# Performance work log

Measured on AMD Instinct MI355X. Metric: run time of the kernel, lower is better.

The kernel has to match this reference:

```python
import jax, jax.numpy as jnp
import numpy as np

H = 128          # h_dim
N_NODES = 100000
N_EDGES = 1600000
N_GRAPHS = 256
EPS_BN = 1e-5


def setup_inputs() -> dict:
    key = jax.random.key(0)
    ks = jax.random.split(key, 12)
    x = jax.random.normal(ks[0], (N_NODES, 4), dtype=jnp.float32)
    edge_index = jax.random.randint(ks[1], (2, N_EDGES), 0, N_NODES, dtype=jnp.int64)
    batch = jnp.sort(jax.random.randint(ks[2], (N_NODES,), 0, N_GRAPHS, dtype=jnp.int64))
    # Linear weights (xavier-ish scale), stored as [in, out]
    W1 = jax.random.normal(ks[3], (4, H), dtype=jnp.float32) * (1.0 / np.sqrt(4))
    W2 = jax.random.normal(ks[4], (H, H), dtype=jnp.float32) * (1.0 / np.sqrt(H))
    W3 = jax.random.normal(ks[5], (H, H), dtype=jnp.float32) * (1.0 / np.sqrt(H))
    Wfc = jax.random.normal(ks[6], (H, 1), dtype=jnp.float32) * (1.0 / np.sqrt(H))
    def bn_params(k):
        k1, k2, k3, k4 = jax.random.split(k, 4)
        gamma = 1.0 + 0.1 * jax.random.normal(k1, (H,), dtype=jnp.float32)
        beta = 0.1 * jax.random.normal(k2, (H,), dtype=jnp.float32)
        mean = 0.1 * jax.random.normal(k3, (H,), dtype=jnp.float32)
        var = 1.0 + 0.1 * jax.random.uniform(k4, (H,), dtype=jnp.float32)
        return gamma, beta, mean, var
    g1, b1, m1, v1 = bn_params(ks[7])
    g2, b2, m2, v2 = bn_params(ks[8])
    g3, b3, m3, v3 = bn_params(ks[9])
    return {
        "x": x, "edge_index": edge_index, "batch": batch,
        "W1": W1, "g1": g1, "b1": b1, "m1": m1, "v1": v1,
        "W2": W2, "g2": g2, "b2": b2, "m2": m2, "v2": v2,
        "W3": W3, "g3": g3, "b3": b3, "m3": m3, "v3": v3,
        "Wfc": Wfc,
    }


def _gin_layer(h, src, dst, W, gamma, beta, mean, var):
    # GINConv with eps=0: mlp(x + sum_{j in N(i)} x_j)
    aggr = jax.ops.segment_sum(h[src], dst, num_segments=N_NODES)
    z = (h + aggr) @ W                                  # Linear(bias=False)
    z = (z - mean) * (gamma / jnp.sqrt(var + EPS_BN)) + beta  # BatchNorm1d (eval)
    return jax.nn.relu(z)


def reference(x, edge_index, batch,
              W1, g1, b1, m1, v1,
              W2, g2, b2, m2, v2,
              W3, g3, b3, m3, v3,
              Wfc):
    src, dst = edge_index[0], edge_index[1]
    h = _gin_layer(x, src, dst, W1, g1, b1, m1, v1)
    h = _gin_layer(h, src, dst, W2, g2, b2, m2, v2)
    h = _gin_layer(h, src, dst, W3, g3, b3, m3, v3)
    # dropout: identity in eval mode
    sums = jax.ops.segment_sum(h, batch, num_segments=N_GRAPHS)      # [G, H]
    cnts = jax.ops.segment_sum(jnp.ones((N_NODES, 1), h.dtype), batch,
                               num_segments=N_GRAPHS)                # [G, 1]
    pooled = sums / jnp.maximum(cnts, 1.0)
    return jax.nn.sigmoid(pooled @ Wfc)                               # [G, 1]
```

## Files before the change

### kernel.cpp

```cpp
#include <hip/hip_runtime.h>
#include <hip/hip_fp8.h>
#include <math.h>

#define N_NODES 100000
#define N_EDGES 1600000
#define N_GRAPHS 256
#define H 128
#define EPS_BN 1e-5f
#define ELLW 64

#define PSZ 256
#define PSH 8
#define P_PART 391
#define BLD_NBLK 200
#define EPT 32
#define EPB_A (256 * EPT)

typedef unsigned int uint;
typedef unsigned short ushort;
typedef __attribute__((ext_vector_type(8))) short bf16x8;
typedef __attribute__((ext_vector_type(4))) float f32x4;
typedef __attribute__((ext_vector_type(2))) float f32x2;
typedef __attribute__((ext_vector_type(4))) int i32x4;
typedef __attribute__((ext_vector_type(2))) int i32x2;

__device__ __forceinline__ uint f2bf_bits(float x) {
    uint u = __float_as_uint(x);
    return (u + 0x7fffu + ((u >> 16) & 1u)) >> 16;
}
__device__ __forceinline__ uint pack_bf2(float a, float b) {
    return f2bf_bits(a) | (f2bf_bits(b) << 16);
}

__device__ __forceinline__ unsigned char f32_to_fp8(float x) {
#if __has_builtin(__builtin_amdgcn_cvt_pk_fp8_f32)
    int v = __builtin_amdgcn_cvt_pk_fp8_f32(x, 0.0f, 0, false);
    return (unsigned char)(v & 0xff);
#else
    __hip_fp8_e4m3 q(x);
    return (unsigned char)q.__x;
#endif
}
__device__ __forceinline__ f32x4 fp8x4_to_f32x4(uint v) {
    f32x4 r;
#if __has_builtin(__builtin_amdgcn_cvt_pk_f32_fp8)
    f32x2 lo = __builtin_amdgcn_cvt_pk_f32_fp8((int)v, false);
    f32x2 hi = __builtin_amdgcn_cvt_pk_f32_fp8((int)v, true);
    r.x = lo.x; r.y = lo.y; r.z = hi.x; r.w = hi.y;
#else
    __hip_fp8_e4m3 a, b, c, d;
    a.__x = (unsigned char)(v & 0xff);
    b.__x = (unsigned char)((v >> 8) & 0xff);
    c.__x = (unsigned char)((v >> 16) & 0xff);
    d.__x = (unsigned char)((v >> 24) & 0xff);
    r.x = (float)a; r.y = (float)b; r.z = (float)c; r.w = (float)d;
#endif
    return r;
}

__global__ __launch_bounds__(256) void k_hist(const int* __restrict__ dst,
                                              int* __restrict__ hist,
                                              const int* __restrict__ batch,
                                              int* __restrict__ gstart,
                                              const float* __restrict__ W2,
                                              ushort* __restrict__ Wpk2,
                                              const float* __restrict__ W3,
                                              ushort* __restrict__ Wpk3,
                                              float* __restrict__ Gz,
                                              uint* __restrict__ Hf8pad) {
    __shared__ int h[P_PART];
    int b = blockIdx.x;
    if (b < BLD_NBLK) {
        for (int i = threadIdx.x; i < P_PART; i += 256) h[i] = 0;
        __syncthreads();
        int base = b * EPB_A + threadIdx.x * EPT;
        #pragma unroll
        for (int j = 0; j < EPT / 4; j++) {
            int e = base + j * 4;
            if (e + 4 <= N_EDGES) {
                i32x4 d = __builtin_nontemporal_load((const i32x4*)&dst[e]);
                atomicAdd(&h[d.x >> PSH], 1);
                atomicAdd(&h[d.y >> PSH], 1);
                atomicAdd(&h[d.z >> PSH], 1);
                atomicAdd(&h[d.w >> PSH], 1);
            }
        }
        __syncthreads();
        for (int i = threadIdx.x; i < P_PART; i += 256)
            hist[b * P_PART + i] = h[i];
        return;
    }
    if (b < 592) {
        int n = (b - 200) * 256 + threadIdx.x;
        if (n >= N_NODES) return;
        int g = batch[n];
        int gp = (n == 0) ? -1 : batch[n - 1];
        for (int gr = gp + 1; gr <= g; gr++) gstart[gr] = n;
        if (n == N_NODES - 1) {
            for (int gr = g + 1; gr <= N_GRAPHS; gr++) gstart[gr] = N_NODES;
        }
        return;
    }
    if (b >= 608) {
        if (threadIdx.x < N_GRAPHS) Gz[threadIdx.x] = 0.0f;
        if (threadIdx.x < 32) Hf8pad[threadIdx.x] = 0u;
        return;
    }
    const float* W = (b < 600) ? W2 : W3;
    ushort* Wpk = (b < 600) ? Wpk2 : Wpk3;
    int t = ((b < 600) ? (b - 592) : (b - 600)) * 256 + threadIdx.x;
    int lane = t & 63, nt = (t >> 6) & 7, kt = t >> 9;
    int n = nt * 16 + (lane & 15);
    int kbase = kt * 32 + (lane >> 4) * 8;
    ushort v[8];
    #pragma unroll
    for (int j = 0; j < 8; j++)
        v[j] = (ushort)f2bf_bits(W[(size_t)(kbase + j) * H + n]);
    uint4 pk;
    pk.x = (uint)v[0] | ((uint)v[1] << 16);
    pk.y = (uint)v[2] | ((uint)v[3] << 16);
    pk.z = (uint)v[4] | ((uint)v[5] << 16);
    pk.w = (uint)v[6] | ((uint)v[7] << 16);
    *(uint4*)&Wpk[(size_t)t * 8] = pk;
}

__global__ __launch_bounds__(256) void k_scan_a(const int* __restrict__ hist,
                                                int* __restrict__ offs,
                                                int* __restrict__ tot) {
    __shared__ int lds[256];
    int p = blockIdx.x;
    int t = threadIdx.x;
    int v = (t < BLD_NBLK) ? hist[t * P_PART + p] : 0;
    lds[t] = v;
    __syncthreads();
    for (int off = 1; off < 256; off <<= 1) {
        int tmp = (t >= off) ? lds[t - off] : 0;
        __syncthreads();
        lds[t] += tmp;
        __syncthreads();
    }
    if (t < BLD_NBLK) offs[t * P_PART + p] = lds[t] - v;
    if (t == 255) tot[p] = lds[255];
}

__global__ void k_scan_b(const int* __restrict__ tot, int* __restrict__ parr) {
    __shared__ int lds[512];
    int p = threadIdx.x;
    int v = (p < P_PART) ? tot[p] : 0;
    lds[p] = v;
    __syncthreads();
    for (int off = 1; off < 512; off <<= 1) {
        int tmp = (p >= off) ? lds[p - off] : 0;
        __syncthreads();
        lds[p] += tmp;
        __syncthreads();
    }
    if (p < P_PART) parr[p] = lds[p] - v;
    if (p == 0) parr[P_PART] = N_EDGES;
}

__global__ __launch_bounds__(256) void k_scatter(const int* __restrict__ src,
                                                 const int* __restrict__ dst,
                                                 const int* __restrict__ offs,
                                                 const int* __restrict__ parr,
                                                 i32x2* __restrict__ ebuf) {
    __shared__ int lofs[P_PART];
    for (int i = threadIdx.x; i < P_PART; i += 256)
        lofs[i] = offs[blockIdx.x * P_PART + i] + parr[i];
    __syncthreads();
    int base = blockIdx.x * EPB_A + threadIdx.x * EPT;
    #pragma unroll
    for (int j = 0; j < EPT / 4; j++) {
        int e = base + j * 4;
        if (e + 4 <= N_EDGES) {
            i32x4 d = __builtin_nontemporal_load((const i32x4*)&dst[e]);
            i32x4 s = __builtin_nontemporal_load((const i32x4*)&src[e]);
            #pragma unroll
            for (int k = 0; k < 4; k++) {
                int dk = (k == 0) ? d.x : (k == 1) ? d.y : (k == 2) ? d.z : d.w;
                int sk = (k == 0) ? s.x : (k == 1) ? s.y : (k == 2) ? s.z : s.w;
                int pos = atomicAdd(&lofs[dk >> PSH], 1);
                i32x2 sd; sd.x = sk; sd.y = dk;
                ebuf[pos] = sd;
            }
        }
    }
}

__global__ __launch_bounds__(256) void k_build(const i32x2* __restrict__ ebuf,
                                               const int* __restrict__ parr,
                                               int* __restrict__ cnt,
                                               int* __restrict__ ell) {
    __shared__ int lc[PSZ];
    int p = blockIdx.x;
    for (int i = threadIdx.x; i < PSZ; i += 256) lc[i] = 0;
    __syncthreads();
    int e0 = parr[p], e1 = parr[p + 1];
    for (int i = e0 + threadIdx.x; i < e1; i += 256) {
        i32x2 sd = ebuf[i];
        int d = sd.y;
        int slot = atomicAdd(&lc[d & (PSZ - 1)], 1);
        if (slot < ELLW) ell[(size_t)d * ELLW + slot] = sd.x;
    }
    __syncthreads();
    int nb = p * PSZ;
    for (int i = threadIdx.x; i < PSZ; i += 256) {
        int n = nb + i;
        if (n < N_NODES) {
            int c = lc[i];
            cnt[n] = c;
            int cc = (c < ELLW) ? c : ELLW;
            int cp = (cc + 15) & ~15;
            if (cp > ELLW) cp = ELLW;
            for (int slot = cc; slot < cp; slot++)
                ell[(size_t)n * ELLW + slot] = N_NODES;
        }
    }
}

__global__ __launch_bounds__(256) void k_layer1(
    const float* __restrict__ x, const int* __restrict__ cnt,
    const int* __restrict__ ell, const float* __restrict__ W1,
    const float* __restrict__ gamma, const float* __restrict__ beta,
    const float* __restrict__ mean, const float* __restrict__ var,
    uint* __restrict__ Hf8) {
    __shared__ float scs[128], shs[128];
    int tid = threadIdx.x;
    if (tid < 128) {
        float sc = gamma[tid] * rsqrtf(var[tid] + EPS_BN);
        scs[tid] = sc;
        shs[tid] = beta[tid] - mean[tid] * sc;
    }
    __syncthreads();
    int lane = tid & 63, wave = tid >> 6;
    int sub = lane >> 4, m = lane & 15;
    int n = blockIdx.x * 16 + wave * 4 + sub;
    if (n >= N_NODES) return;
    int cn = cnt[n]; if (cn > ELLW) cn = ELLW;
    const int* row = &ell[(size_t)n * ELLW];
    const char* xb = (const char*)x;
    float4 acc = {0.f, 0.f, 0.f, 0.f};
    for (int e = m; e < cn; e += 16) {
        float4 v = *(const float4*)(xb + ((uint)row[e] << 4));
        acc.x += v.x; acc.y += v.y; acc.z += v.z; acc.w += v.w;
    }
    #pragma unroll
    for (int off = 8; off > 0; off >>= 1) {
        acc.x += __shfl_down(acc.x, off, 16);
        acc.y += __shfl_down(acc.y, off, 16);
        acc.z += __shfl_down(acc.z, off, 16);
        acc.w += __shfl_down(acc.w, off, 16);
    }
    int src = lane & 48;
    float4 xs = *(const float4*)(xb + ((uint)n << 4));
    float uu[4];
    uu[0] = __shfl(acc.x, src, 64) + xs.x;
    uu[1] = __shfl(acc.y, src, 64) + xs.y;
    uu[2] = __shfl(acc.z, src, 64) + xs.z;
    uu[3] = __shfl(acc.w, src, 64) + xs.w;
    int j0 = m * 8;
    float z[8] = {0.f, 0.f, 0.f, 0.f, 0.f, 0.f, 0.f, 0.f};
    #pragma unroll
    for (int k = 0; k < 4; k++) {
        float4 wa = *(const float4*)&W1[k * H + j0];
        float4 wb = *(const float4*)&W1[k * H + j0 + 4];
        z[0] += uu[k] * wa.x; z[1] += uu[k] * wa.y;
        z[2] += uu[k] * wa.z; z[3] += uu[k] * wa.w;
        z[4] += uu[k] * wb.x; z[5] += uu[k] * wb.y;
        z[6] += uu[k] * wb.z; z[7] += uu[k] * wb.w;
    }
    #pragma unroll
    for (int i = 0; i < 8; i++)
        z[i] = fmaxf(z[i] * scs[j0 + i] + shs[j0 + i], 0.0f);
    uint2 q;
    q.x = (uint)f32_to_fp8(z[0]) | ((uint)f32_to_fp8(z[1]) << 8)
        | ((uint)f32_to_fp8(z[2]) << 16) | ((uint)f32_to_fp8(z[3]) << 24);
    q.y = (uint)f32_to_fp8(z[4]) | ((uint)f32_to_fp8(z[5]) << 8)
        | ((uint)f32_to_fp8(z[6]) << 16) | ((uint)f32_to_fp8(z[7]) << 24);
    *(uint2*)&Hf8[(size_t)n * 32 + m * 2] = q;
}

__global__ __launch_bounds__(256) void k_aggr128(
    const uint* __restrict__ Hf8, const int* __restrict__ cnt,
    const int* __restrict__ ell, uint* __restrict__ Ubf) {
    int t = blockIdx.x * 256 + threadIdx.x;
    int n = t >> 6, lane = t & 63;
    if (n >= N_NODES) return;
    int g = lane >> 4, c8 = lane & 15;
    const int* row = &ell[(size_t)n * ELLW];
    const char* Hb = (const char*)Hf8;
    uint co = (uint)c8 << 3;
    i32x4 id = *(const i32x4*)(row + 4 * g);
    uint2 sp = {0u, 0u};
    if (g == 0) sp = *(const uint2*)(Hb + (((uint)n << 7) | co));
    int cn = cnt[n]; if (cn > ELLW) cn = ELLW;
    int cnp = (cn + 15) & ~15; if (cnp > ELLW) cnp = ELLW;

    f32x4 A = {0.f, 0.f, 0.f, 0.f};
    f32x4 B = {0.f, 0.f, 0.f, 0.f};
    for (int e = 0; e < cnp; e += 16) {
        i32x4 idn = id;
        if (e + 16 < cnp) idn = *(const i32x4*)(row + e + 16 + 4 * g);
        uint2 p0 = *(const uint2*)(Hb + (((uint)id.x << 7) | co));
        uint2 p1 = *(const uint2*)(Hb + (((uint)id.y << 7) | co));
        uint2 p2 = *(const uint2*)(Hb + (((uint)id.z << 7) | co));
        uint2 p3 = *(const uint2*)(Hb + (((uint)id.w << 7) | co));
        f32x4 l0 = fp8x4_to_f32x4(p0.x), h0 = fp8x4_to_f32x4(p0.y);
        f32x4 l1 = fp8x4_to_f32x4(p1.x), h1 = fp8x4_to_f32x4(p1.y);
        f32x4 l2 = fp8x4_to_f32x4(p2.x), h2 = fp8x4_to_f32x4(p2.y);
        f32x4 l3 = fp8x4_to_f32x4(p3.x), h3 = fp8x4_to_f32x4(p3.y);
        A += (l0 + l1) + (l2 + l3);
        B += (h0 + h1) + (h2 + h3);
        id = idn;
    }
    if (g == 0) {
        A += fp8x4_to_f32x4(sp.x);
        B += fp8x4_to_f32x4(sp.y);
    }
    #pragma unroll
    for (int off = 32; off >= 16; off >>= 1) {
        A.x += __shfl_down(A.x, off, 64);
        A.y += __shfl_down(A.y, off, 64);
        A.z += __shfl_down(A.z, off, 64);
        A.w += __shfl_down(A.w, off, 64);
        B.x += __shfl_down(B.x, off, 64);
        B.y += __shfl_down(B.y, off, 64);
        B.z += __shfl_down(B.z, off, 64);
        B.w += __shfl_down(B.w, off, 64);
    }
    if (g == 0) {
        uint4 ov;
        ov.x = pack_bf2(A.x, A.y);
        ov.y = pack_bf2(A.z, A.w);
        ov.z = pack_bf2(B.x, B.y);
        ov.w = pack_bf2(B.z, B.w);
        *(uint4*)&Ubf[(size_t)n * 64 + c8 * 4] = ov;
    }
}

__global__ __launch_bounds__(256) void k_gemm_mfma(
    const uint* __restrict__ Ubf, const uint* __restrict__ Wpk,
    const float* __restrict__ gamma, const float* __restrict__ beta,
    const float* __restrict__ mean, const float* __restrict__ var,
    unsigned char* __restrict__ Hf8,
    const int* __restrict__ batch, const float* __restrict__ Wfc,
    float* __restrict__ Gz, int mode) {
    __shared__ uint lds_u[64 * 68];
    __shared__ float wfc[128];
    __shared__ int bb[64];
    __shared__ float sblk[64];
    int tid = threadIdx.x;
    int row0 = blockIdx.x * 64;
    if (mode == 2) {
        if (tid < 128) wfc[tid] = Wfc[tid];
        if (tid < 64) {
            int rr = row0 + tid;
            bb[tid] = (rr < N_NODES) ? batch[rr] : -1;
        }
    }
    #pragma unroll
    for (int it = 0; it < 4; it++) {
        int r = it * 16 + (tid >> 4);
        int c = (tid & 15) * 4;
        int gr = row0 + r; if (gr >= N_NODES) gr = N_NODES - 1;
        uint4 v = *(const uint4*)&Ubf[(size_t)gr * 64 + c];
        *(uint4*)&lds_u[r * 68 + c] = v;
    }
    __syncthreads();

    int wave = tid >> 6, lane = tid & 63;
    int m = lane & 15, quad = lane >> 4;
    bf16x8 a[4];
    #pragma unroll
    for (int kt = 0; kt < 4; kt++)
        a[kt] = *(const bf16x8*)&lds_u[(wave * 16 + m) * 68 + kt * 16 + quad * 4];

    f32x4 acc[8];
    #pragma unroll
    for (int nt = 0; nt < 8; nt++) acc[nt] = (f32x4){0.f, 0.f, 0.f, 0.f};

    #pragma unroll
    for (int nt = 0; nt < 8; nt++) {
        #pragma unroll
        for (int kt = 0; kt < 4; kt++) {
            bf16x8 b = *(const bf16x8*)&Wpk[((size_t)(kt * 8 + nt) * 64 + lane) * 4];
            acc[nt] = __builtin_amdgcn_mfma_f32_16x16x32_bf16(a[kt], b, acc[nt], 0, 0, 0);
        }
    }

    if (mode == 1) {
        #pragma unroll
        for (int nt = 0; nt < 8; nt++) {
            int col = nt * 16 + m;
            float sc = gamma[col] * rsqrtf(var[col] + EPS_BN);
            float sh = beta[col] - mean[col] * sc;
            #pragma unroll
            for (int r = 0; r < 4; r++) {
                int row = row0 + wave * 16 + quad * 4 + r;
                if (row < N_NODES) {
                    float z = fmaxf(acc[nt][r] * sc + sh, 0.0f);
                    Hf8[(size_t)row * 128 + col] = f32_to_fp8(z);
                }
            }
        }
    } else {
        float pr[4] = {0.f, 0.f, 0.f, 0.f};
        #pragma unroll
        for (int nt = 0; nt < 8; nt++) {
            int col = nt * 16 + m;
            float sc = gamma[col] * rsqrtf(var[col] + EPS_BN);
            float sh = beta[col] - mean[col] * sc;
            float wf = wfc[col];
            #pragma unroll
            for (int r = 0; r < 4; r++) {
                float z = fmaxf(acc[nt][r] * sc + sh, 0.0f);
                pr[r] += z * wf;
            }
        }
        #pragma unroll
        for (int r = 0; r < 4; r++) {
            float p = pr[r];
            p += __shfl_down(p, 8, 16);
            p += __shfl_down(p, 4, 16);
            p += __shfl_down(p, 2, 16);
            p += __shfl_down(p, 1, 16);
            if (m == 0) sblk[wave * 16 + quad * 4 + r] = p;
        }
        __syncthreads();
        if (tid == 0) {
            int i = 0;
            while (i < 64 && row0 + i < N_NODES) {
                int g = bb[i];
                float s = 0.0f;
                while (i < 64 && row0 + i < N_NODES && bb[i] == g) {
                    s += sblk[i]; i++;
                }
                atomicAdd(&Gz[g], s);
            }
        }
    }
}

__global__ void k_fc(const float* __restrict__ Gz, const int* __restrict__ gstart,
                     float* __restrict__ out) {
    int g = threadIdx.x;
    if (g < N_GRAPHS) {
        int c = gstart[g + 1] - gstart[g];
        float z = Gz[g] / fmaxf((float)c, 1.0f);
        out[g] = 1.0f / (1.0f + expf(-z));
    }
}

extern "C" void kernel_launch(void* const* d_in, const int* in_sizes, int n_in,
                              void* d_out, int out_size, void* d_ws, size_t ws_size,
                              hipStream_t stream) {
    const float* x     = (const float*)d_in[0];
    const int*   ei    = (const int*)d_in[1];
    const int*   batch = (const int*)d_in[2];
    const float* W1    = (const float*)d_in[3];
    const float* g1    = (const float*)d_in[4];
    const float* b1    = (const float*)d_in[5];
    const float* m1    = (const float*)d_in[6];
    const float* v1    = (const float*)d_in[7];
    const float* W2    = (const float*)d_in[8];
    const float* g2    = (const float*)d_in[9];
    const float* b2    = (const float*)d_in[10];
    const float* m2    = (const float*)d_in[11];
    const float* v2    = (const float*)d_in[12];
    const float* W3    = (const float*)d_in[13];
    const float* g3    = (const float*)d_in[14];
    const float* b3    = (const float*)d_in[15];
    const float* m3    = (const float*)d_in[16];
    const float* v3    = (const float*)d_in[17];
    const float* Wfc   = (const float*)d_in[18];
    float* out = (float*)d_out;

    const int* srcp = ei;
    const int* dstp = ei + N_EDGES;

    uint* Ubf  = (uint*)d_ws;
    uint* Hf8u = Ubf + (size_t)N_NODES * 64;
    int* cnt   = (int*)(Hf8u + (size_t)N_NODES * 32 + 32);
    int* ell   = cnt + N_NODES;
    int* gstart = ell + (size_t)N_NODES * ELLW;
    ushort* Wpk2 = (ushort*)(gstart + 260);
    ushort* Wpk3 = Wpk2 + 16384;
    int* hist  = (int*)(Wpk3 + 16384);
    int* offs  = hist + BLD_NBLK * P_PART;
    int* parr  = offs + BLD_NBLK * P_PART;
    int* tot   = parr + 400;
    float* Gz  = (float*)(tot + 400);
    i32x2* ebuf = (i32x2*)Ubf;
    uint* Hf8pad = Hf8u + (size_t)N_NODES * 32;

    k_hist<<<609, 256, 0, stream>>>(dstp, hist, batch, gstart, W2, Wpk2, W3, Wpk3,
                                    Gz, Hf8pad);
    k_scan_a<<<P_PART, 256, 0, stream>>>(hist, offs, tot);
    k_scan_b<<<1, 512, 0, stream>>>(tot, parr);
    k_scatter<<<BLD_NBLK, 256, 0, stream>>>(srcp, dstp, offs, parr, ebuf);
    k_build<<<P_PART, 256, 0, stream>>>(ebuf, parr, cnt, ell);

    k_layer1<<<(N_NODES + 15) / 16, 256, 0, stream>>>(
        x, cnt, ell, W1, g1, b1, m1, v1, Hf8u);
    k_aggr128<<<(N_NODES * 64 + 255) / 256, 256, 0, stream>>>(Hf8u, cnt, ell, Ubf);
    k_gemm_mfma<<<(N_NODES + 63) / 64, 256, 0, stream>>>(
        Ubf, (const uint*)Wpk2, g2, b2, m2, v2, (unsigned char*)Hf8u,
        batch, Wfc, Gz, 1);
    k_aggr128<<<(N_NODES * 64 + 255) / 256, 256, 0, stream>>>(Hf8u, cnt, ell, Ubf);
    k_gemm_mfma<<<(N_NODES + 63) / 64, 256, 0, stream>>>(
        Ubf, (const uint*)Wpk3, g3, b3, m3, v3, (unsigned char*)Hf8u,
        batch, Wfc, Gz, 2);
    k_fc<<<1, 256, 0, stream>>>(Gz, gstart, out);
}
```

Measured before the change: 274.9 us.

## Raise edge-sort block count, pack edge buffer entries, precompute BN scale in LDS

Result: no change. 271.6 us, median of 2 (-1.2%).

```diff
diff --git a/kernel.cpp b/kernel.cpp
--- a/kernel.cpp
+++ b/kernel.cpp
@@ -12,9 +12,9 @@
 #define PSZ 256
 #define PSH 8
 #define P_PART 391
-#define BLD_NBLK 200
-#define EPT 32
-#define EPB_A (256 * EPT)
+#define NB_BLD 782
+#define EPT_B 8
+#define EPB_B (256 * EPT_B)
 
 typedef unsigned int uint;
 typedef unsigned short ushort;
@@ -22,7 +22,6 @@
 typedef __attribute__((ext_vector_type(4))) float f32x4;
 typedef __attribute__((ext_vector_type(2))) float f32x2;
 typedef __attribute__((ext_vector_type(4))) int i32x4;
-typedef __attribute__((ext_vector_type(2))) int i32x2;
 
 __device__ __forceinline__ uint f2bf_bits(float x) {
     uint u = __float_as_uint(x);
@@ -70,12 +69,12 @@
                                               uint* __restrict__ Hf8pad) {
     __shared__ int h[P_PART];
     int b = blockIdx.x;
-    if (b < BLD_NBLK) {
+    if (b < NB_BLD) {
         for (int i = threadIdx.x; i < P_PART; i += 256) h[i] = 0;
         __syncthreads();
-        int base = b * EPB_A + threadIdx.x * EPT;
+        int base = b * EPB_B + threadIdx.x * EPT_B;
         #pragma unroll
-        for (int j = 0; j < EPT / 4; j++) {
+        for (int j = 0; j < EPT_B / 4; j++) {
             int e = base + j * 4;
             if (e + 4 <= N_EDGES) {
                 i32x4 d = __builtin_nontemporal_load((const i32x4*)&dst[e]);
@@ -90,8 +89,8 @@
             hist[b * P_PART + i] = h[i];
         return;
     }
-    if (b < 592) {
-        int n = (b - 200) * 256 + threadIdx.x;
+    if (b < 1174) {
+        int n = (b - NB_BLD) * 256 + threadIdx.x;
         if (n >= N_NODES) return;
         int g = batch[n];
         int gp = (n == 0) ? -1 : batch[n - 1];
@@ -101,14 +100,14 @@
         }
         return;
     }
-    if (b >= 608) {
+    if (b >= 1190) {
         if (threadIdx.x < N_GRAPHS) Gz[threadIdx.x] = 0.0f;
         if (threadIdx.x < 32) Hf8pad[threadIdx.x] = 0u;
         return;
     }
-    const float* W = (b < 600) ? W2 : W3;
-    ushort* Wpk = (b < 600) ? Wpk2 : Wpk3;
-    int t = ((b < 600) ? (b - 592) : (b - 600)) * 256 + threadIdx.x;
+    const float* W = (b < 1182) ? W2 : W3;
+    ushort* Wpk = (b < 1182) ? Wpk2 : Wpk3;
+    int t = ((b < 1182) ? (b - 1174) : (b - 1182)) * 256 + threadIdx.x;
     int lane = t & 63, nt = (t >> 6) & 7, kt = t >> 9;
     int n = nt * 16 + (lane & 15);
     int kbase = kt * 32 + (lane >> 4) * 8;
@@ -130,8 +129,14 @@
     __shared__ int lds[256];
     int p = blockIdx.x;
     int t = threadIdx.x;
-    int v = (t < BLD_NBLK) ? hist[t * P_PART + p] : 0;
-    lds[t] = v;
+    int v0 = 0, v1 = 0, v2 = 0, v3 = 0;
+    int b0 = t * 4;
+    if (b0 + 0 < NB_BLD) v0 = hist[(b0 + 0) * P_PART + p];
+    if (b0 + 1 < NB_BLD) v1 = hist[(b0 + 1) * P_PART + p];
+    if (b0 + 2 < NB_BLD) v2 = hist[(b0 + 2) * P_PART + p];
+    if (b0 + 3 < NB_BLD) v3 = hist[(b0 + 3) * P_PART + p];
+    int tt = v0 + v1 + v2 + v3;
+    lds[t] = tt;
     __syncthreads();
     for (int off = 1; off < 256; off <<= 1) {
         int tmp = (t >= off) ? lds[t - off] : 0;
@@ -139,7 +144,11 @@
         lds[t] += tmp;
         __syncthreads();
     }
-    if (t < BLD_NBLK) offs[t * P_PART + p] = lds[t] - v;
+    int run = lds[t] - tt;
+    if (b0 + 0 < NB_BLD) { offs[(b0 + 0) * P_PART + p] = run; run += v0; }
+    if (b0 + 1 < NB_BLD) { offs[(b0 + 1) * P_PART + p] = run; run += v1; }
+    if (b0 + 2 < NB_BLD) { offs[(b0 + 2) * P_PART + p] = run; run += v2; }
+    if (b0 + 3 < NB_BLD) { offs[(b0 + 3) * P_PART + p] = run; run += v3; }
     if (t == 255) tot[p] = lds[255];
 }
 
@@ -163,14 +172,14 @@
                                                  const int* __restrict__ dst,
                                                  const int* __restrict__ offs,
                                                  const int* __restrict__ parr,
-                                                 i32x2* __restrict__ ebuf) {
+                                                 uint* __restrict__ ebuf) {
     __shared__ int lofs[P_PART];
     for (int i = threadIdx.x; i < P_PART; i += 256)
         lofs[i] = offs[blockIdx.x * P_PART + i] + parr[i];
     __syncthreads();
-    int base = blockIdx.x * EPB_A + threadIdx.x * EPT;
-    #pragma unroll
-    for (int j = 0; j < EPT / 4; j++) {
+    int base = blockIdx.x * EPB_B + threadIdx.x * EPT_B;
+    #pragma unroll
+    for (int j = 0; j < EPT_B / 4; j++) {
         int e = base + j * 4;
         if (e + 4 <= N_EDGES) {
             i32x4 d = __builtin_nontemporal_load((const i32x4*)&dst[e]);
@@ -180,14 +189,13 @@
                 int dk = (k == 0) ? d.x : (k == 1) ? d.y : (k == 2) ? d.z : d.w;
                 int sk = (k == 0) ? s.x : (k == 1) ? s.y : (k == 2) ? s.z : s.w;
                 int pos = atomicAdd(&lofs[dk >> PSH], 1);
-                i32x2 sd; sd.x = sk; sd.y = dk;
-                ebuf[pos] = sd;
+                ebuf[pos] = ((uint)sk << 8) | ((uint)dk & 255u);
             }
         }
     }
 }
 
-__global__ __launch_bounds__(256) void k_build(const i32x2* __restrict__ ebuf,
+__global__ __launch_bounds__(256) void k_build(const uint* __restrict__ ebuf,
                                                const int* __restrict__ parr,
                                                int* __restrict__ cnt,
                                                int* __restrict__ ell) {
@@ -196,14 +204,14 @@
     for (int i = threadIdx.x; i < PSZ; i += 256) lc[i] = 0;
     __syncthreads();
     int e0 = parr[p], e1 = parr[p + 1];
+    int nb = p * PSZ;
     for (int i = e0 + threadIdx.x; i < e1; i += 256) {
-        i32x2 sd = ebuf[i];
-        int d = sd.y;
-        int slot = atomicAdd(&lc[d & (PSZ - 1)], 1);
-        if (slot < ELLW) ell[(size_t)d * ELLW + slot] = sd.x;
-    }
-    __syncthreads();
-    int nb = p * PSZ;
+        uint sd = ebuf[i];
+        int dl = (int)(sd & 255u);
+        int slot = atomicAdd(&lc[dl], 1);
+        if (slot < ELLW) ell[(size_t)(nb + dl) * ELLW + slot] = (int)(sd >> 8);
+    }
+    __syncthreads();
     for (int i = threadIdx.x; i < PSZ; i += 256) {
         int n = nb + i;
         if (n < N_NODES) {
@@ -346,11 +354,17 @@
     const int* __restrict__ batch, const float* __restrict__ Wfc,
     float* __restrict__ Gz, int mode) {
     __shared__ uint lds_u[64 * 68];
+    __shared__ float sc_s[128], sh_s[128];
     __shared__ float wfc[128];
     __shared__ int bb[64];
     __shared__ float sblk[64];
     int tid = threadIdx.x;
     int row0 = blockIdx.x * 64;
+    if (tid < 128) {
+        float sc = gamma[tid] * rsqrtf(var[tid] + EPS_BN);
+        sc_s[tid] = sc;
+        sh_s[tid] = beta[tid] - mean[tid] * sc;
+    }
     if (mode == 2) {
         if (tid < 128) wfc[tid] = Wfc[tid];
         if (tid < 64) {
@@ -392,8 +406,7 @@
         #pragma unroll
         for (int nt = 0; nt < 8; nt++) {
             int col = nt * 16 + m;
-            float sc = gamma[col] * rsqrtf(var[col] + EPS_BN);
-            float sh = beta[col] - mean[col] * sc;
+            float sc = sc_s[col], sh = sh_s[col];
             #pragma unroll
             for (int r = 0; r < 4; r++) {
                 int row = row0 + wave * 16 + quad * 4 + r;
@@ -408,8 +421,7 @@
         #pragma unroll
         for (int nt = 0; nt < 8; nt++) {
             int col = nt * 16 + m;
-            float sc = gamma[col] * rsqrtf(var[col] + EPS_BN);
-            float sh = beta[col] - mean[col] * sc;
+            float sc = sc_s[col], sh = sh_s[col];
             float wf = wfc[col];
             #pragma unroll
             for (int r = 0; r < 4; r++) {
@@ -486,18 +498,18 @@
     ushort* Wpk2 = (ushort*)(gstart + 260);
     ushort* Wpk3 = Wpk2 + 16384;
     int* hist  = (int*)(Wpk3 + 16384);
-    int* offs  = hist + BLD_NBLK * P_PART;
-    int* parr  = offs + BLD_NBLK * P_PART;
+    int* offs  = hist + NB_BLD * P_PART;
+    int* parr  = offs + NB_BLD * P_PART;
     int* tot   = parr + 400;
     float* Gz  = (float*)(tot + 400);
-    i32x2* ebuf = (i32x2*)Ubf;
+    uint* ebuf = Ubf;
     uint* Hf8pad = Hf8u + (size_t)N_NODES * 32;
 
-    k_hist<<<609, 256, 0, stream>>>(dstp, hist, batch, gstart, W2, Wpk2, W3, Wpk3,
-                                    Gz, Hf8pad);
+    k_hist<<<1191, 256, 0, stream>>>(dstp, hist, batch, gstart, W2, Wpk2, W3, Wpk3,
+                                     Gz, Hf8pad);
     k_scan_a<<<P_PART, 256, 0, stream>>>(hist, offs, tot);
     k_scan_b<<<1, 512, 0, stream>>>(tot, parr);
-    k_scatter<<<BLD_NBLK, 256, 0, stream>>>(srcp, dstp, offs, parr, ebuf);
+    k_scatter<<<NB_BLD, 256, 0, stream>>>(srcp, dstp, offs, parr, ebuf);
     k_build<<<P_PART, 256, 0, stream>>>(ebuf, parr, cnt, ell);
 
     k_layer1<<<(N_NODES + 15) / 16, 256, 0, stream>>>(
```
